# Optimization experiments

Measured on AMD Instinct MI355X. Metric: run time of the kernel, lower is better.

## Reference

```python
import jax, jax.numpy as jnp
import numpy as np
from jax import lax

T, N, F, H, E = 8, 20000, 128, 256, 320000
LEAK = 0.9


def setup_inputs() -> dict:
    key = jax.random.key(0)
    k = jax.random.split(key, 7)
    x = jax.random.normal(k[0], (T, N, F), dtype=jnp.float32)
    edge_index = jax.random.randint(k[1], (2, E), 0, N, dtype=jnp.int32)
    # reservoir weights, scaled ~1/sqrt(fan_in) so tanh stays in its active range
    w_in0 = jax.random.normal(k[2], (H, F), dtype=jnp.float32) / jnp.sqrt(F)
    w_rec0 = jax.random.normal(k[3], (H, H), dtype=jnp.float32) / jnp.sqrt(H)
    w_in1 = jax.random.normal(k[4], (H, H), dtype=jnp.float32) / jnp.sqrt(H)
    w_rec1 = jax.random.normal(k[5], (H, H), dtype=jnp.float32) / jnp.sqrt(H)
    leakage = jnp.array(LEAK, dtype=jnp.float32)
    return {"x": x, "edge_index": edge_index, "w_in0": w_in0, "w_rec0": w_rec0,
            "w_in1": w_in1, "w_rec1": w_rec1, "leakage": leakage}


def reference(x, edge_index, w_in0, w_rec0, w_in1, w_rec1, leakage):
    # DynamicGraphReservoir with 2 ReservoirConvLayers, fixed graph over time,
    # zero initial states, no pooling, fully=False, return_sequences=False.
    src, dst = edge_index[0], edge_index[1]
    num_nodes = x.shape[1]

    def layer(w_in, w_rec, inp, state):
        # neighbour aggregation: sum_{(j->i) in E} state[j]   (scatter-add)
        agg = jax.ops.segment_sum(state[src], dst, num_segments=num_nodes)
        return leakage * jnp.tanh(inp @ w_in.T + agg @ w_rec.T) + (1.0 - leakage) * state

    def step(states, xt):
        s0, s1 = states
        s0 = layer(w_in0, w_rec0, xt, s0)   # layer 0 consumes input signal
        s1 = layer(w_in1, w_rec1, s0, s1)   # layer 1 consumes layer-0 state
        return (s0, s1), None

    init = (jnp.zeros((num_nodes, w_rec0.shape[0]), x.dtype),
            jnp.zeros((num_nodes, w_rec1.shape[0]), x.dtype))
    (s0, s1), _ = lax.scan(step, init, x)
    return s1  # final-layer final state: (nodes, hidden)
```

## Files before the change

### kernel.cpp

```cpp
#include <hip/hip_runtime.h>
#include <math.h>

#define T_STEPS 8
#define N_NODES 20000
#define F_IN    128
#define H_DIM   256
#define E_EDGES 320000

typedef __attribute__((ext_vector_type(8))) short short8;
typedef __attribute__((ext_vector_type(4))) float f32x4;

__device__ __forceinline__ void split2(float v, unsigned short& h, unsigned short& l) {
    unsigned vi = __float_as_uint(v);
    h = (unsigned short)(vi >> 16);
    float hf = __uint_as_float(vi & 0xffff0000u);
    l = (unsigned short)(__float_as_uint(v - hf) >> 16);
}


__global__ void count_kernel(const int* __restrict__ dst, int* __restrict__ counts, int E) {
    int e = blockIdx.x * blockDim.x + threadIdx.x;
    if (e < E) atomicAdd(&counts[dst[e]], 1);
}

__global__ void scan_kernel(const int* __restrict__ counts, int* __restrict__ row_ptr,
                            int* __restrict__ cursors, int n) {
    __shared__ int buf[1024];
    __shared__ int carry_s;
    int tid = threadIdx.x;
    if (tid == 0) carry_s = 0;
    __syncthreads();
    for (int base = 0; base < n; base += 1024) {
        int i = base + tid;
        int v = (i < n) ? counts[i] : 0;
        buf[tid] = v;
        __syncthreads();
        for (int off = 1; off < 1024; off <<= 1) {
            int t = (tid >= off) ? buf[tid - off] : 0;
            __syncthreads();
            buf[tid] += t;
            __syncthreads();
        }
        int incl = buf[tid];
        int carry = carry_s;
        if (i < n) {
            int ex = carry + incl - v;
            row_ptr[i] = ex;
            cursors[i] = ex;
        }
        __syncthreads();
        if (tid == 1023) carry_s = carry + incl;
        __syncthreads();
    }
    if (tid == 0) row_ptr[n] = carry_s;
}

__global__ void fill_kernel(const int* __restrict__ src, const int* __restrict__ dst,
                            int* __restrict__ cursors, int* __restrict__ col, int E) {
    int e = blockIdx.x * blockDim.x + threadIdx.x;
    if (e < E) {
        int d = dst[e];
        int p = atomicAdd(&cursors[d], 1);
        col[p] = src[e];
    }
}


__global__ void cvt_frag(const float* __restrict__ W, int K,
                         unsigned short* __restrict__ fh, unsigned short* __restrict__ fl) {
    int g = blockIdx.x * 256 + threadIdx.x;
    int KP32 = K >> 5;
    int total = (H_DIM / 16) * KP32 * 64;
    if (g >= total) return;
    int lane = g & 63;
    int kp = (g >> 6) % KP32;
    int rt = g / (KP32 << 6);
    int r = rt * 16 + (lane & 15);
    int c = kp * 32 + (lane >> 4) * 8;
    const float* p = W + (size_t)r * K + c;
    short8 h, l;
    #pragma unroll
    for (int j = 0; j < 8; ++j) {
        unsigned short hh, ll;
        split2(p[j], hh, ll);
        h[j] = (short)hh; l[j] = (short)ll;
    }
    *(short8*)(fh + (size_t)g * 8) = h;
    *(short8*)(fl + (size_t)g * 8) = l;
}


__global__ __launch_bounds__(256) void gather2_kernel(
        const float* __restrict__ s0, const float* __restrict__ s1,
        const int* __restrict__ row_ptr, const int* __restrict__ col,
        float* __restrict__ agg0, float* __restrict__ agg1, int n) {
    const float* s  = blockIdx.y ? s1 : s0;
    float*       ag = blockIdx.y ? agg1 : agg0;
    int wv = threadIdx.x >> 6, lane = threadIdx.x & 63;
    int node = blockIdx.x * 4 + wv;
    if (node >= n) return;
    int beg = row_ptr[node], end = row_ptr[node + 1];
    const float4* s4 = (const float4*)s;
    float ax = 0.f, ay = 0.f, az = 0.f, aw = 0.f;
    float bx = 0.f, by = 0.f, bz = 0.f, bw = 0.f;
    int j = beg;
    for (; j + 1 < end; j += 2) {
        int c0 = col[j], c1 = col[j + 1];
        float4 v0 = s4[(size_t)c0 * 64 + lane];
        float4 v1 = s4[(size_t)c1 * 64 + lane];
        ax += v0.x; ay += v0.y; az += v0.z; aw += v0.w;
        bx += v1.x; by += v1.y; bz += v1.z; bw += v1.w;
    }
    if (j < end) {
        int c = col[j];
        float4 v = s4[(size_t)c * 64 + lane];
        ax += v.x; ay += v.y; az += v.z; aw += v.w;
    }
    float4 o;
    o.x = ax + bx; o.y = ay + by; o.z = az + bz; o.w = aw + bw;
    ((float4*)ag)[(size_t)node * 64 + lane] = o;
}


__global__ __launch_bounds__(256) void update_mfma(
        const float* __restrict__ A1, int K1,
        const float* __restrict__ A2,
        const unsigned short* __restrict__ B1h, const unsigned short* __restrict__ B1l,
        const unsigned short* __restrict__ B2h, const unsigned short* __restrict__ B2l,
        const float* __restrict__ s_old, float* __restrict__ s_out,
        const float* __restrict__ leak_ptr) {
    const int tid = threadIdx.x;
    const int lane = tid & 63, w = tid >> 6;
    const int fr = lane & 15, fq = lane >> 4;
    const int m0 = blockIdx.x * 32;
    const int wn = w * 64;
    const int rtbase = wn >> 4;

    f32x4 acc[2][4];
    #pragma unroll
    for (int mi = 0; mi < 2; ++mi)
        #pragma unroll
        for (int nt = 0; nt < 4; ++nt)
            acc[mi][nt] = (f32x4){0.f, 0.f, 0.f, 0.f};

    #pragma unroll 1
    for (int part = 0; part < 2; ++part) {
        const float* Af; int K;
        const unsigned short *Bh, *Bl;
        if (part == 0) { Af = A1; K = K1; Bh = B1h; Bl = B1l; }
        else {
            if (!A2) break;
            Af = A2; K = H_DIM; Bh = B2h; Bl = B2l;
        }
        const int KP32 = K >> 5;
        #pragma unroll 1
        for (int kp = 0; kp < KP32; ++kp) {
            short8 ah[2], al[2];
            #pragma unroll
            for (int mi = 0; mi < 2; ++mi) {
                const float* ap = Af + (size_t)(m0 + mi * 16 + fr) * K + kp * 32 + fq * 8;
                float4 v0 = *(const float4*)ap;
                float4 v1 = *(const float4*)(ap + 4);
                unsigned short h, l;
                split2(v0.x, h, l); ah[mi][0] = (short)h; al[mi][0] = (short)l;
                split2(v0.y, h, l); ah[mi][1] = (short)h; al[mi][1] = (short)l;
                split2(v0.z, h, l); ah[mi][2] = (short)h; al[mi][2] = (short)l;
                split2(v0.w, h, l); ah[mi][3] = (short)h; al[mi][3] = (short)l;
                split2(v1.x, h, l); ah[mi][4] = (short)h; al[mi][4] = (short)l;
                split2(v1.y, h, l); ah[mi][5] = (short)h; al[mi][5] = (short)l;
                split2(v1.z, h, l); ah[mi][6] = (short)h; al[mi][6] = (short)l;
                split2(v1.w, h, l); ah[mi][7] = (short)h; al[mi][7] = (short)l;
            }
            short8 bh[4], bl[4];
            #pragma unroll
            for (int nt = 0; nt < 4; ++nt) {
                size_t off = ((size_t)((rtbase + nt) * KP32 + kp) * 64 + lane) * 8;
                bh[nt] = *(const short8*)(Bh + off);
                bl[nt] = *(const short8*)(Bl + off);
            }
            #pragma unroll
            for (int mi = 0; mi < 2; ++mi)
                #pragma unroll
                for (int nt = 0; nt < 4; ++nt) {
                    f32x4 c = acc[mi][nt];
                    c = __builtin_amdgcn_mfma_f32_16x16x32_bf16(ah[mi], bh[nt], c, 0, 0, 0);
                    c = __builtin_amdgcn_mfma_f32_16x16x32_bf16(al[mi], bh[nt], c, 0, 0, 0);
                    c = __builtin_amdgcn_mfma_f32_16x16x32_bf16(ah[mi], bl[nt], c, 0, 0, 0);
                    acc[mi][nt] = c;
                }
        }
    }

    const float leak = leak_ptr[0], il = 1.0f - leak;
    #pragma unroll
    for (int mi = 0; mi < 2; ++mi)
        #pragma unroll
        for (int r = 0; r < 4; ++r) {
            int m = m0 + mi * 16 + fq * 4 + r;
            #pragma unroll
            for (int nt = 0; nt < 4; ++nt) {
                int n = wn + nt * 16 + fr;
                size_t idx = (size_t)m * H_DIM + n;
                float old = s_old[idx];
                float pre = acc[mi][nt][r];
                float e = __expf(2.0f * pre);
                float th = 1.0f - 2.0f / (e + 1.0f);
                s_out[idx] = leak * th + il * old;
            }
        }
}


extern "C" void kernel_launch(void* const* d_in, const int* in_sizes, int n_in,
                              void* d_out, int out_size, void* d_ws, size_t ws_size,
                              hipStream_t stream) {
    const float* x        = (const float*)d_in[0];
    const int*   edge     = (const int*)d_in[1];
    const float* w_in0    = (const float*)d_in[2];
    const float* w_rec0   = (const float*)d_in[3];
    const float* w_in1    = (const float*)d_in[4];
    const float* w_rec1   = (const float*)d_in[5];
    const float* leak_ptr = (const float*)d_in[6];

    const int* src = edge;
    const int* dst = edge + E_EDGES;

    float* s1 = (float*)d_out;

    char* ws = (char*)d_ws;
    size_t off = 0;
    auto alloc = [&](size_t bytes) -> char* {
        char* p = ws + off;
        off += (bytes + 255) & ~(size_t)255;
        return p;
    };
    const size_t state_bytes = (size_t)N_NODES * H_DIM * sizeof(float);
    float* s0   = (float*)alloc(state_bytes);
    float* agg0 = (float*)alloc(state_bytes);
    float* agg1 = (float*)alloc(state_bytes);
    unsigned short* w0h  = (unsigned short*)alloc(256 * 128 * 2);
    unsigned short* w0l  = (unsigned short*)alloc(256 * 128 * 2);
    unsigned short* wr0h = (unsigned short*)alloc(256 * 256 * 2);
    unsigned short* wr0l = (unsigned short*)alloc(256 * 256 * 2);
    unsigned short* w1h  = (unsigned short*)alloc(256 * 256 * 2);
    unsigned short* w1l  = (unsigned short*)alloc(256 * 256 * 2);
    unsigned short* wr1h = (unsigned short*)alloc(256 * 256 * 2);
    unsigned short* wr1l = (unsigned short*)alloc(256 * 256 * 2);
    int* row_ptr = (int*)alloc((N_NODES + 1) * sizeof(int));
    int* cursors = (int*)alloc(N_NODES * sizeof(int));
    int* counts  = (int*)alloc(N_NODES * sizeof(int));
    int* col     = (int*)alloc((size_t)E_EDGES * sizeof(int));

    hipMemsetAsync(s0, 0, state_bytes, stream);
    hipMemsetAsync(s1, 0, state_bytes, stream);
    hipMemsetAsync(counts, 0, N_NODES * sizeof(int), stream);

    cvt_frag<<<16, 256, 0, stream>>>(w_in0, F_IN, w0h, w0l);
    cvt_frag<<<32, 256, 0, stream>>>(w_rec0, H_DIM, wr0h, wr0l);
    cvt_frag<<<32, 256, 0, stream>>>(w_in1, H_DIM, w1h, w1l);
    cvt_frag<<<32, 256, 0, stream>>>(w_rec1, H_DIM, wr1h, wr1l);

    count_kernel<<<(E_EDGES + 255) / 256, 256, 0, stream>>>(dst, counts, E_EDGES);
    scan_kernel<<<1, 1024, 0, stream>>>(counts, row_ptr, cursors, N_NODES);
    fill_kernel<<<(E_EDGES + 255) / 256, 256, 0, stream>>>(src, dst, cursors, col, E_EDGES);

    dim3 ggrid(N_NODES / 4, 2);
    dim3 ugrid(N_NODES / 32);

    for (int t = 0; t < T_STEPS; ++t) {
        const float* xt = x + (size_t)t * N_NODES * F_IN;
        if (t == 0) {
            update_mfma<<<ugrid, 256, 0, stream>>>(
                xt, F_IN, nullptr, w0h, w0l, nullptr, nullptr,
                s0, s0, leak_ptr);
            update_mfma<<<ugrid, 256, 0, stream>>>(
                s0, H_DIM, nullptr, w1h, w1l, nullptr, nullptr,
                s1, s1, leak_ptr);
        } else {
            gather2_kernel<<<ggrid, 256, 0, stream>>>(s0, s1, row_ptr, col,
                                                      agg0, agg1, N_NODES);
            update_mfma<<<ugrid, 256, 0, stream>>>(
                xt, F_IN, agg0, w0h, w0l, wr0h, wr0l,
                s0, s0, leak_ptr);
            update_mfma<<<ugrid, 256, 0, stream>>>(
                s0, H_DIM, agg1, w1h, w1l, wr1h, wr1l,
                s1, s1, leak_ptr);
        }
    }
}
```

Before: 1.364 ms.

## Fuse neighbour gather into MFMA update kernel via shared memory with double-buffered states

Drops the separate gather kernel. Each update block now aggregates the neighbour states for its 32 rows into an LDS tile, then runs the recurrent matmul straight from shared memory. State buffers are ping-ponged so the gather can read the previous state while the new one is written, arranged so the final state lands in the output. This removes the global write and read of the two aggregate arrays and one launch per step. In exchange the gather now runs serially inside each GEMM block, and 33KB of LDS per block may lower occupancy.

New measurement: 1.265 ms. 1.08x faster.

```diff
diff --git a/kernel.cpp b/kernel.cpp
--- a/kernel.cpp
+++ b/kernel.cpp
@@ -90,51 +90,57 @@
 }
 
 
-__global__ __launch_bounds__(256) void gather2_kernel(
-        const float* __restrict__ s0, const float* __restrict__ s1,
-        const int* __restrict__ row_ptr, const int* __restrict__ col,
-        float* __restrict__ agg0, float* __restrict__ agg1, int n) {
-    const float* s  = blockIdx.y ? s1 : s0;
-    float*       ag = blockIdx.y ? agg1 : agg0;
-    int wv = threadIdx.x >> 6, lane = threadIdx.x & 63;
-    int node = blockIdx.x * 4 + wv;
-    if (node >= n) return;
-    int beg = row_ptr[node], end = row_ptr[node + 1];
-    const float4* s4 = (const float4*)s;
-    float ax = 0.f, ay = 0.f, az = 0.f, aw = 0.f;
-    float bx = 0.f, by = 0.f, bz = 0.f, bw = 0.f;
-    int j = beg;
-    for (; j + 1 < end; j += 2) {
-        int c0 = col[j], c1 = col[j + 1];
-        float4 v0 = s4[(size_t)c0 * 64 + lane];
-        float4 v1 = s4[(size_t)c1 * 64 + lane];
-        ax += v0.x; ay += v0.y; az += v0.z; aw += v0.w;
-        bx += v1.x; by += v1.y; bz += v1.z; bw += v1.w;
-    }
-    if (j < end) {
-        int c = col[j];
-        float4 v = s4[(size_t)c * 64 + lane];
-        ax += v.x; ay += v.y; az += v.z; aw += v.w;
-    }
-    float4 o;
-    o.x = ax + bx; o.y = ay + by; o.z = az + bz; o.w = aw + bw;
-    ((float4*)ag)[(size_t)node * 64 + lane] = o;
-}
-
-
-__global__ __launch_bounds__(256) void update_mfma(
+__global__ __launch_bounds__(256) void fused_update(
         const float* __restrict__ A1, int K1,
-        const float* __restrict__ A2,
+        const float* __restrict__ s_prev,
         const unsigned short* __restrict__ B1h, const unsigned short* __restrict__ B1l,
         const unsigned short* __restrict__ B2h, const unsigned short* __restrict__ B2l,
-        const float* __restrict__ s_old, float* __restrict__ s_out,
-        const float* __restrict__ leak_ptr) {
+        float* __restrict__ s_new,
+        const int* __restrict__ row_ptr, const int* __restrict__ col,
+        const float* __restrict__ leak_ptr, int do_gather) {
+    __shared__ float aggs[32][260];
     const int tid = threadIdx.x;
     const int lane = tid & 63, w = tid >> 6;
     const int fr = lane & 15, fq = lane >> 4;
     const int m0 = blockIdx.x * 32;
     const int wn = w * 64;
-    const int rtbase = wn >> 4;
+    const int rtbase = w * 4;
+
+    if (do_gather) {
+        const float4* s4 = (const float4*)s_prev;
+        #pragma unroll 1
+        for (int i = 0; i < 8; ++i) {
+            int r = w * 8 + i;
+            int beg = row_ptr[m0 + r], end = row_ptr[m0 + r + 1];
+            float x0 = 0.f, y0 = 0.f, z0 = 0.f, w0 = 0.f;
+            float x1 = 0.f, y1 = 0.f, z1 = 0.f, w1 = 0.f;
+            float x2 = 0.f, y2 = 0.f, z2 = 0.f, w2 = 0.f;
+            float x3 = 0.f, y3 = 0.f, z3 = 0.f, w3 = 0.f;
+            int j = beg;
+            for (; j + 3 < end; j += 4) {
+                int c0 = col[j], c1 = col[j + 1], c2 = col[j + 2], c3 = col[j + 3];
+                float4 v0 = s4[(size_t)c0 * 64 + lane];
+                float4 v1 = s4[(size_t)c1 * 64 + lane];
+                float4 v2 = s4[(size_t)c2 * 64 + lane];
+                float4 v3 = s4[(size_t)c3 * 64 + lane];
+                x0 += v0.x; y0 += v0.y; z0 += v0.z; w0 += v0.w;
+                x1 += v1.x; y1 += v1.y; z1 += v1.z; w1 += v1.w;
+                x2 += v2.x; y2 += v2.y; z2 += v2.z; w2 += v2.w;
+                x3 += v3.x; y3 += v3.y; z3 += v3.z; w3 += v3.w;
+            }
+            for (; j < end; ++j) {
+                float4 v = s4[(size_t)col[j] * 64 + lane];
+                x0 += v.x; y0 += v.y; z0 += v.z; w0 += v.w;
+            }
+            float4 t;
+            t.x = (x0 + x1) + (x2 + x3);
+            t.y = (y0 + y1) + (y2 + y3);
+            t.z = (z0 + z1) + (z2 + z3);
+            t.w = (w0 + w1) + (w2 + w3);
+            *(float4*)&aggs[r][lane * 4] = t;
+        }
+        __syncthreads();
+    }
 
     f32x4 acc[2][4];
     #pragma unroll
@@ -143,22 +149,14 @@
         for (int nt = 0; nt < 4; ++nt)
             acc[mi][nt] = (f32x4){0.f, 0.f, 0.f, 0.f};
 
-    #pragma unroll 1
-    for (int part = 0; part < 2; ++part) {
-        const float* Af; int K;
-        const unsigned short *Bh, *Bl;
-        if (part == 0) { Af = A1; K = K1; Bh = B1h; Bl = B1l; }
-        else {
-            if (!A2) break;
-            Af = A2; K = H_DIM; Bh = B2h; Bl = B2l;
-        }
-        const int KP32 = K >> 5;
+    {
+        const int KP32 = K1 >> 5;
         #pragma unroll 1
         for (int kp = 0; kp < KP32; ++kp) {
             short8 ah[2], al[2];
             #pragma unroll
             for (int mi = 0; mi < 2; ++mi) {
-                const float* ap = Af + (size_t)(m0 + mi * 16 + fr) * K + kp * 32 + fq * 8;
+                const float* ap = A1 + (size_t)(m0 + mi * 16 + fr) * K1 + kp * 32 + fq * 8;
                 float4 v0 = *(const float4*)ap;
                 float4 v1 = *(const float4*)(ap + 4);
                 unsigned short h, l;
@@ -175,8 +173,8 @@
             #pragma unroll
             for (int nt = 0; nt < 4; ++nt) {
                 size_t off = ((size_t)((rtbase + nt) * KP32 + kp) * 64 + lane) * 8;
-                bh[nt] = *(const short8*)(Bh + off);
-                bl[nt] = *(const short8*)(Bl + off);
+                bh[nt] = *(const short8*)(B1h + off);
+                bl[nt] = *(const short8*)(B1l + off);
             }
             #pragma unroll
             for (int mi = 0; mi < 2; ++mi)
@@ -191,6 +189,45 @@
         }
     }
 
+    if (B2h) {
+        #pragma unroll 1
+        for (int kp = 0; kp < 8; ++kp) {
+            short8 ah[2], al[2];
+            #pragma unroll
+            for (int mi = 0; mi < 2; ++mi) {
+                const float* ap = &aggs[mi * 16 + fr][kp * 32 + fq * 8];
+                float4 v0 = *(const float4*)ap;
+                float4 v1 = *(const float4*)(ap + 4);
+                unsigned short h, l;
+                split2(v0.x, h, l); ah[mi][0] = (short)h; al[mi][0] = (short)l;
+                split2(v0.y, h, l); ah[mi][1] = (short)h; al[mi][1] = (short)l;
+                split2(v0.z, h, l); ah[mi][2] = (short)h; al[mi][2] = (short)l;
+                split2(v0.w, h, l); ah[mi][3] = (short)h; al[mi][3] = (short)l;
+                split2(v1.x, h, l); ah[mi][4] = (short)h; al[mi][4] = (short)l;
+                split2(v1.y, h, l); ah[mi][5] = (short)h; al[mi][5] = (short)l;
+                split2(v1.z, h, l); ah[mi][6] = (short)h; al[mi][6] = (short)l;
+                split2(v1.w, h, l); ah[mi][7] = (short)h; al[mi][7] = (short)l;
+            }
+            short8 bh[4], bl[4];
+            #pragma unroll
+            for (int nt = 0; nt < 4; ++nt) {
+                size_t off = ((size_t)((rtbase + nt) * 8 + kp) * 64 + lane) * 8;
+                bh[nt] = *(const short8*)(B2h + off);
+                bl[nt] = *(const short8*)(B2l + off);
+            }
+            #pragma unroll
+            for (int mi = 0; mi < 2; ++mi)
+                #pragma unroll
+                for (int nt = 0; nt < 4; ++nt) {
+                    f32x4 c = acc[mi][nt];
+                    c = __builtin_amdgcn_mfma_f32_16x16x32_bf16(ah[mi], bh[nt], c, 0, 0, 0);
+                    c = __builtin_amdgcn_mfma_f32_16x16x32_bf16(al[mi], bh[nt], c, 0, 0, 0);
+                    c = __builtin_amdgcn_mfma_f32_16x16x32_bf16(ah[mi], bl[nt], c, 0, 0, 0);
+                    acc[mi][nt] = c;
+                }
+        }
+    }
+
     const float leak = leak_ptr[0], il = 1.0f - leak;
     #pragma unroll
     for (int mi = 0; mi < 2; ++mi)
@@ -201,11 +238,11 @@
             for (int nt = 0; nt < 4; ++nt) {
                 int n = wn + nt * 16 + fr;
                 size_t idx = (size_t)m * H_DIM + n;
-                float old = s_old[idx];
+                float old = s_prev[idx];
                 float pre = acc[mi][nt][r];
                 float e = __expf(2.0f * pre);
                 float th = 1.0f - 2.0f / (e + 1.0f);
-                s_out[idx] = leak * th + il * old;
+                s_new[idx] = leak * th + il * old;
             }
         }
 }
@@ -225,8 +262,6 @@
     const int* src = edge;
     const int* dst = edge + E_EDGES;
 
-    float* s1 = (float*)d_out;
-
     char* ws = (char*)d_ws;
     size_t off = 0;
     auto alloc = [&](size_t bytes) -> char* {
@@ -235,9 +270,11 @@
         return p;
     };
     const size_t state_bytes = (size_t)N_NODES * H_DIM * sizeof(float);
-    float* s0   = (float*)alloc(state_bytes);
-    float* agg0 = (float*)alloc(state_bytes);
-    float* agg1 = (float*)alloc(state_bytes);
+    float* s0b[2]; float* s1b[2];
+    s0b[0] = (float*)alloc(state_bytes);
+    s0b[1] = (float*)alloc(state_bytes);
+    s1b[0] = (float*)d_out;
+    s1b[1] = (float*)alloc(state_bytes);
     unsigned short* w0h  = (unsigned short*)alloc(256 * 128 * 2);
     unsigned short* w0l  = (unsigned short*)alloc(256 * 128 * 2);
     unsigned short* wr0h = (unsigned short*)alloc(256 * 256 * 2);
@@ -251,8 +288,8 @@
     int* counts  = (int*)alloc(N_NODES * sizeof(int));
     int* col     = (int*)alloc((size_t)E_EDGES * sizeof(int));
 
-    hipMemsetAsync(s0, 0, state_bytes, stream);
-    hipMemsetAsync(s1, 0, state_bytes, stream);
+    hipMemsetAsync(s0b[0], 0, state_bytes, stream);
+    hipMemsetAsync(s1b[0], 0, state_bytes, stream);
     hipMemsetAsync(counts, 0, N_NODES * sizeof(int), stream);
 
     cvt_frag<<<16, 256, 0, stream>>>(w_in0, F_IN, w0h, w0l);
@@ -264,27 +301,19 @@
     scan_kernel<<<1, 1024, 0, stream>>>(counts, row_ptr, cursors, N_NODES);
     fill_kernel<<<(E_EDGES + 255) / 256, 256, 0, stream>>>(src, dst, cursors, col, E_EDGES);
 
-    dim3 ggrid(N_NODES / 4, 2);
     dim3 ugrid(N_NODES / 32);
 
     for (int t = 0; t < T_STEPS; ++t) {
         const float* xt = x + (size_t)t * N_NODES * F_IN;
-        if (t == 0) {
-            update_mfma<<<ugrid, 256, 0, stream>>>(
-                xt, F_IN, nullptr, w0h, w0l, nullptr, nullptr,
-                s0, s0, leak_ptr);
-            update_mfma<<<ugrid, 256, 0, stream>>>(
-                s0, H_DIM, nullptr, w1h, w1l, nullptr, nullptr,
-                s1, s1, leak_ptr);
-        } else {
-            gather2_kernel<<<ggrid, 256, 0, stream>>>(s0, s1, row_ptr, col,
-                                                      agg0, agg1, N_NODES);
-            update_mfma<<<ugrid, 256, 0, stream>>>(
-                xt, F_IN, agg0, w0h, w0l, wr0h, wr0l,
-                s0, s0, leak_ptr);
-            update_mfma<<<ugrid, 256, 0, stream>>>(
-                s0, H_DIM, agg1, w1h, w1l, wr1h, wr1l,
-                s1, s1, leak_ptr);
-        }
-    }
-}
+        int rd = t & 1, wr = rd ^ 1;
+        int dg = (t > 0) ? 1 : 0;
+        fused_update<<<ugrid, 256, 0, stream>>>(
+            xt, F_IN, s0b[rd],
+            w0h, w0l, dg ? wr0h : nullptr, dg ? wr0l : nullptr,
+            s0b[wr], row_ptr, col, leak_ptr, dg);
+        fused_update<<<ugrid, 256, 0, stream>>>(
+            s0b[wr], H_DIM, s1b[rd],
+            w1h, w1l, dg ? wr1h : nullptr, dg ? wr1l : nullptr,
+            s1b[wr], row_ptr, col, leak_ptr, dg);
+    }
+}
```
